# Optimization experiments

Measured on AMD Instinct MI355X. Metric: run time of the kernel, lower is better.

Reference implementation:

```python
import jax, jax.numpy as jnp
import numpy as np

KERNEL_SIZE = 128
NEG_INF = -1e30


def setup_inputs() -> dict:
    key = jax.random.key(0)
    ks = jax.random.split(key, 5)
    B, S, D, H = 4, 4096, 512, 512
    x = jax.random.normal(ks[0], (B, S, D), dtype=jnp.float32)
    # torch nn.Linear weights: [out_features, in_features], y = x @ W.T + b
    Wq_w = jax.random.normal(ks[1], (H, D), dtype=jnp.float32) * (1.0 / np.sqrt(D))
    Wq_b = jax.random.normal(ks[2], (H,), dtype=jnp.float32) * 0.01
    Wk_w = jax.random.normal(ks[3], (H, D), dtype=jnp.float32) * (1.0 / np.sqrt(D))
    Wk_b = jax.random.normal(ks[4], (H,), dtype=jnp.float32) * 0.01
    return {"x": x, "Wq_w": Wq_w, "Wq_b": Wq_b, "Wk_w": Wk_w, "Wk_b": Wk_b}


def reference(x, Wq_w, Wq_b, Wk_w, Wk_b):
    # q, k: [B, S, H]
    q = jnp.einsum('bsd,hd->bsh', x, Wq_w) + Wq_b
    k = jnp.einsum('bsd,hd->bsh', x, Wk_w) + Wk_b
    # dense scores [B, S, S]
    scores = jnp.einsum('bih,bjh->bij', q, k)
    # band mask: True where i-kernel_size+1 <= j <= i+kernel_size-1
    idx = jnp.arange(x.shape[1])
    band = jnp.abs(idx[:, None] - idx[None, :]) < KERNEL_SIZE  # [S, S]
    scores = jnp.where(band[None, :, :], scores, NEG_INF)
    attn = jax.nn.softmax(scores, axis=2)
    # attend over raw x (no V projection in original module)
    return jnp.einsum('bij,bjd->bid', attn, x)
```

## Files before the change

### kernel.cpp

```cpp
#include <hip/hip_runtime.h>
#include <hip/hip_bf16.h>

#define S_LEN 4096
#define NEG_INF_F (-1e30f)

typedef __attribute__((ext_vector_type(4))) float f32x4;
typedef __attribute__((ext_vector_type(8))) short s16x8;
typedef unsigned short u16;

static __device__ __forceinline__ u16 f2bf(float f) {
    unsigned u = __builtin_bit_cast(unsigned, f);
    unsigned r = u + 0x7FFFu + ((u >> 16) & 1u);
    return (u16)(r >> 16);
}
static __device__ __forceinline__ float bf2f(u16 h) {
    unsigned u = ((unsigned)h) << 16;
    return __builtin_bit_cast(float, u);
}
static __device__ __forceinline__ void split4(const float4 v, ushort4& hi, ushort4& lo) {
    hi.x = f2bf(v.x); lo.x = f2bf(v.x - bf2f(hi.x));
    hi.y = f2bf(v.y); lo.y = f2bf(v.y - bf2f(hi.y));
    hi.z = f2bf(v.z); lo.z = f2bf(v.z - bf2f(hi.z));
    hi.w = f2bf(v.w); lo.w = f2bf(v.w - bf2f(hi.w));
}
static __device__ __forceinline__ void gl_lds16(const void* g, void* l) {
    __builtin_amdgcn_global_load_lds(
        (const __attribute__((address_space(1))) void*)g,
        (__attribute__((address_space(3))) void*)l, 16, 0, 0);
}
static __device__ __forceinline__ int swz64(int row, int col_u16) {
    return row * 64 + (col_u16 ^ ((row & 7) << 3));
}
static __device__ __forceinline__ int swz32(int row, int col_u16) {
    return row * 32 + (col_u16 ^ (((row >> 1) & 3) << 3));
}
static __device__ __forceinline__ int swz320(int row, int col_u16) {
    return row * 320 + (col_u16 ^ ((row & 7) << 3));
}
static __device__ __forceinline__ int xcd_swz512(int bid) {
    return (bid & 7) * 64 + (bid >> 3);
}
static __device__ __forceinline__ int xcd_swz256(int bid) {
    return (bid & 7) * 32 + (bid >> 3);
}

__global__ __launch_bounds__(256) void split_xt_kernel(
    const float* __restrict__ x, u16* __restrict__ xh, u16* __restrict__ xl,
    u16* __restrict__ xT) {
    const int bid = blockIdx.x;
    const int dt = bid & 7, st = (bid >> 3) & 63, b = bid >> 9;
    const int s0 = st * 64, d0 = dt * 64;
    __shared__ u16 T[64][72];
    const int tid = threadIdx.x;
    #pragma unroll
    for (int i = 0; i < 4; ++i) {
        int idx = i * 256 + tid;
        int r = idx >> 4, c4 = (idx & 15) * 4;
        float4 v = *(const float4*)(x + (size_t)(b * S_LEN + s0 + r) * 512 + d0 + c4);
        ushort4 hi, lo; split4(v, hi, lo);
        *(ushort4*)(xh + (size_t)(b * S_LEN + s0 + r) * 512 + d0 + c4) = hi;
        *(ushort4*)(xl + (size_t)(b * S_LEN + s0 + r) * 512 + d0 + c4) = lo;
        *(ushort4*)&T[r][c4] = hi;
    }
    __syncthreads();
    #pragma unroll
    for (int i = 0; i < 2; ++i) {
        int idx = i * 256 + tid;
        int dr = idx >> 3, sc = idx & 7;
        s16x8 v;
        #pragma unroll
        for (int t = 0; t < 8; ++t) v[t] = (short)T[sc * 8 + t][dr];
        *(s16x8*)&xT[(size_t)(b * 512 + d0 + dr) * S_LEN + s0 + sc * 8] = v;
    }
}

__global__ __launch_bounds__(256) void mt_kernel(
    const float* __restrict__ Wk, const float* __restrict__ Wq,
    u16* __restrict__ Mth, u16* __restrict__ Mtl) {
    const int bm = blockIdx.x & 15, bn = blockIdx.x >> 4;
    const int m0 = bm * 32, n0 = bn * 32;
    __shared__ __align__(16) u16 Ath[32 * 72], Atl[32 * 72];
    __shared__ __align__(16) u16 Bth[32 * 72], Btl[32 * 72];
    const int tid = threadIdx.x, lane = tid & 63, w = tid >> 6;
    const int rg = w >> 1, cg = w & 1;
    const int frow = lane & 15, fk = (lane >> 4) * 8;
    f32x4 acc = {};

    for (int h0 = 0; h0 < 512; h0 += 64) {
        #pragma unroll
        for (int i = 0; i < 2; ++i) {
            int idx = i * 256 + tid;
            int h = idx >> 3, c4 = (idx & 7) * 4;
            float4 a = *(const float4*)(Wk + (size_t)(h0 + h) * 512 + m0 + c4);
            ushort4 ahi, alo; split4(a, ahi, alo);
            Ath[(c4 + 0) * 72 + h] = ahi.x; Atl[(c4 + 0) * 72 + h] = alo.x;
            Ath[(c4 + 1) * 72 + h] = ahi.y; Atl[(c4 + 1) * 72 + h] = alo.y;
            Ath[(c4 + 2) * 72 + h] = ahi.z; Atl[(c4 + 2) * 72 + h] = alo.z;
            Ath[(c4 + 3) * 72 + h] = ahi.w; Atl[(c4 + 3) * 72 + h] = alo.w;
            float4 b = *(const float4*)(Wq + (size_t)(h0 + h) * 512 + n0 + c4);
            ushort4 bhi, blo; split4(b, bhi, blo);
            Bth[(c4 + 0) * 72 + h] = bhi.x; Btl[(c4 + 0) * 72 + h] = blo.x;
            Bth[(c4 + 1) * 72 + h] = bhi.y; Btl[(c4 + 1) * 72 + h] = blo.y;
            Bth[(c4 + 2) * 72 + h] = bhi.z; Btl[(c4 + 2) * 72 + h] = blo.z;
            Bth[(c4 + 3) * 72 + h] = bhi.w; Btl[(c4 + 3) * 72 + h] = blo.w;
        }
        __syncthreads();
        #pragma unroll
        for (int kk = 0; kk < 2; ++kk) {
            s16x8 aH = *(const s16x8*)&Ath[(rg * 16 + frow) * 72 + kk * 32 + fk];
            s16x8 aL = *(const s16x8*)&Atl[(rg * 16 + frow) * 72 + kk * 32 + fk];
            s16x8 bH = *(const s16x8*)&Bth[(cg * 16 + frow) * 72 + kk * 32 + fk];
            s16x8 bL = *(const s16x8*)&Btl[(cg * 16 + frow) * 72 + kk * 32 + fk];
            acc = __builtin_amdgcn_mfma_f32_16x16x32_bf16(aH, bH, acc, 0, 0, 0);
            acc = __builtin_amdgcn_mfma_f32_16x16x32_bf16(aH, bL, acc, 0, 0, 0);
            acc = __builtin_amdgcn_mfma_f32_16x16x32_bf16(aL, bH, acc, 0, 0, 0);
        }
        __syncthreads();
    }
    {
        int d1 = n0 + cg * 16 + frow;
        #pragma unroll
        for (int e = 0; e < 4; ++e) {
            int d2 = m0 + rg * 16 + (lane >> 4) * 4 + e;
            float v = acc[e];
            u16 hi = f2bf(v);
            Mth[(size_t)d2 * 512 + d1] = hi;
            Mtl[(size_t)d2 * 512 + d1] = f2bf(v - bf2f(hi));
        }
    }
}

__global__ __launch_bounds__(256) void u_kernel(
    const float* __restrict__ Wk, const float* __restrict__ bq,
    float* __restrict__ u) {
    __shared__ float red[4][64];
    const int tid = threadIdx.x, c = tid & 63, hg = tid >> 6;
    const int d2 = blockIdx.x * 64 + c;
    float acc = 0.f;
    for (int h = hg; h < 512; h += 4) acc += Wk[(size_t)h * 512 + d2] * bq[h];
    red[hg][c] = acc;
    __syncthreads();
    if (hg == 0) u[d2] = red[0][c] + red[1][c] + red[2][c] + red[3][c];
}

__global__ __launch_bounds__(512) void z_kernel(
    const u16* __restrict__ xh, const u16* __restrict__ xl,
    const u16* __restrict__ Mth, const u16* __restrict__ Mtl,
    const float* __restrict__ u, u16* __restrict__ zh, u16* __restrict__ zl) {
    const int w_ = xcd_swz512((int)blockIdx.x);
    const int bm = w_ >> 2, bn = w_ & 3;
    const int m0 = bm * 128, n0 = bn * 128;
    __shared__ __align__(16) u16 Ah[128 * 64], Al[128 * 64];
    __shared__ __align__(16) u16 Bh[128 * 64], Bl[128 * 64];
    const int tid = threadIdx.x, lane = tid & 63, w = tid >> 6;
    const int rg = w >> 2, cg = w & 3;
    const int frow = lane & 15, fk = (lane >> 4) * 8;
    f32x4 acc[4][2] = {};

    for (int k0 = 0; k0 < 512; k0 += 64) {
        #pragma unroll
        for (int i = 0; i < 2; ++i) {
            int idx = i * 512 + tid;
            int r = idx >> 3, c = idx & 7;
            int sc = (c ^ (r & 7)) * 8;
            gl_lds16(xh + (size_t)(m0 + r) * 512 + k0 + sc, &Ah[idx * 8]);
            gl_lds16(xl + (size_t)(m0 + r) * 512 + k0 + sc, &Al[idx * 8]);
            gl_lds16(Mth + (size_t)(n0 + r) * 512 + k0 + sc, &Bh[idx * 8]);
            gl_lds16(Mtl + (size_t)(n0 + r) * 512 + k0 + sc, &Bl[idx * 8]);
        }
        __syncthreads();
        #pragma unroll
        for (int kk = 0; kk < 2; ++kk) {
            s16x8 aH[4], aL[4], bH[2], bL[2];
            #pragma unroll
            for (int mi = 0; mi < 4; ++mi) {
                int row = rg * 64 + mi * 16 + frow;
                aH[mi] = *(const s16x8*)&Ah[swz64(row, kk * 32 + fk)];
                aL[mi] = *(const s16x8*)&Al[swz64(row, kk * 32 + fk)];
            }
            #pragma unroll
            for (int ni = 0; ni < 2; ++ni) {
                int row = cg * 32 + ni * 16 + frow;
                bH[ni] = *(const s16x8*)&Bh[swz64(row, kk * 32 + fk)];
                bL[ni] = *(const s16x8*)&Bl[swz64(row, kk * 32 + fk)];
            }
            #pragma unroll
            for (int mi = 0; mi < 4; ++mi)
                #pragma unroll
                for (int ni = 0; ni < 2; ++ni) {
                    acc[mi][ni] = __builtin_amdgcn_mfma_f32_16x16x32_bf16(aH[mi], bH[ni], acc[mi][ni], 0, 0, 0);
                    acc[mi][ni] = __builtin_amdgcn_mfma_f32_16x16x32_bf16(aH[mi], bL[ni], acc[mi][ni], 0, 0, 0);
                    acc[mi][ni] = __builtin_amdgcn_mfma_f32_16x16x32_bf16(aL[mi], bH[ni], acc[mi][ni], 0, 0, 0);
                }
        }
        __syncthreads();
    }
    #pragma unroll
    for (int ni = 0; ni < 2; ++ni) {
        int col = n0 + cg * 32 + ni * 16 + frow;
        float uv = u[col];
        #pragma unroll
        for (int mi = 0; mi < 4; ++mi) {
            int rbase = m0 + rg * 64 + mi * 16 + (lane >> 4) * 4;
            #pragma unroll
            for (int e = 0; e < 4; ++e) {
                float v = acc[mi][ni][e] + uv;
                u16 hi = f2bf(v);
                zh[(size_t)(rbase + e) * 512 + col] = hi;
                zl[(size_t)(rbase + e) * 512 + col] = f2bf(v - bf2f(hi));
            }
        }
    }
}

__global__ __launch_bounds__(1024, 4) void attn_kernel(
    const u16* __restrict__ zh, const u16* __restrict__ zl,
    const u16* __restrict__ xh, const u16* __restrict__ xl,
    const u16* __restrict__ xT, float* __restrict__ out) {
    const int w_ = xcd_swz256((int)blockIdx.x);
    const int b = w_ >> 6, it = w_ & 63;
    const int i0 = it * 64, j0 = i0 - 128;
    const int mrow0 = b * S_LEN + i0;

    __shared__ __align__(16) u16 smem[40960];

    const int tid = threadIdx.x, lane = tid & 63, w = tid >> 6;
    const int g = w >> 2, q = w & 3;
    const int frow = lane & 15, fk = (lane >> 4) * 8;
    const int tstart = g + q * 4;
    const int nt = (q == 3) ? 5 : 4;
    const size_t qoff = (size_t)(mrow0 + g * 16 + frow) * 512;
    const int rq = (lane >> 4) * 4;

    f32x4 acc[5] = {};
    s16x8 krA[3], krB[3];

    auto kload = [&](int s, s16x8* kr) {
        const int k0 = s * 32;
        #pragma unroll
        for (int i = 0; i < 3; ++i) {
            int f = i * 1024 + tid;
            if (f < 2560) {
                int idx = (f < 1280) ? f : f - 1280;
                int r = idx >> 2, c = idx & 3;
                int j = min(max(j0 + r, 0), S_LEN - 1);
                const u16* src = (f < 1280) ? xh : xl;
                kr[i] = *(const s16x8*)(src + (size_t)(b * S_LEN + j) * 512 + k0 + c * 8);
            }
        }
    };
    auto kwrite = [&](const s16x8* kr, int bufoff) {
        #pragma unroll
        for (int i = 0; i < 3; ++i) {
            int f = i * 1024 + tid;
            if (f < 2560) {
                int idx = (f < 1280) ? f : f - 1280;
                int r = idx >> 2, c = idx & 3;
                int off = bufoff + ((f < 1280) ? 0 : 10240) + swz32(r, c * 8);
                *(s16x8*)&smem[off] = kr[i];
            }
        }
    };
    auto qkstep = [&](int t, int bufoff) {
        const int k0 = t * 32;
        s16x8 zH = *(const s16x8*)(zh + qoff + k0 + fk);
        s16x8 zL = *(const s16x8*)(zl + qoff + k0 + fk);
        __builtin_amdgcn_s_setprio(1);
        #pragma unroll
        for (int tt = 0; tt < 5; ++tt) {
            if (tt < nt) {
                int krow = (tstart + tt) * 16 + frow;
                s16x8 bH = *(const s16x8*)&smem[bufoff + swz32(krow, fk)];
                s16x8 bL = *(const s16x8*)&smem[bufoff + 10240 + swz32(krow, fk)];
                acc[tt] = __builtin_amdgcn_mfma_f32_16x16x32_bf16(zH, bH, acc[tt], 0, 0, 0);
                acc[tt] = __builtin_amdgcn_mfma_f32_16x16x32_bf16(zH, bL, acc[tt], 0, 0, 0);
                acc[tt] = __builtin_amdgcn_mfma_f32_16x16x32_bf16(zL, bH, acc[tt], 0, 0, 0);
            }
        }
        __builtin_amdgcn_s_setprio(0);
    };

    kload(0, krA);
    kwrite(krA, 0);
    kload(1, krB);
    __syncthreads();
    for (int tt2 = 0; tt2 < 16; tt2 += 2) {
        if (tt2 + 1 < 16) kwrite(krB, 20480);
        if (tt2 + 2 < 16) kload(tt2 + 2, krA);
        qkstep(tt2, 0);
        __syncthreads();
        if (tt2 + 1 < 16) {
            if (tt2 + 2 < 16) kwrite(krA, 0);
            if (tt2 + 3 < 16) kload(tt2 + 3, krB);
            qkstep(tt2 + 1, 20480);
            __syncthreads();
        }
    }

    float* sred_max = (float*)&smem[20480];
    float* sred_sum = sred_max + 256;
    #pragma unroll
    for (int e = 0; e < 4; ++e) {
        int r = g * 16 + rq + e;
        float m = NEG_INF_F;
        #pragma unroll
        for (int tt = 0; tt < 5; ++tt) {
            if (tt < nt) {
                int jj = (tstart + tt) * 16 + frow;
                int dj = jj - r, j = j0 + jj;
                if (dj >= 1 && dj <= 255 && j >= 0 && j < S_LEN) m = fmaxf(m, acc[tt][e]);
            }
        }
        #pragma unroll
        for (int d = 1; d < 16; d <<= 1) m = fmaxf(m, __shfl_xor(m, d));
        if (frow == 0) sred_max[r * 4 + q] = m;
    }
    __syncthreads();
    float sh[4];
    #pragma unroll
    for (int e = 0; e < 4; ++e) {
        int r = g * 16 + rq + e;
        float mx = fmaxf(fmaxf(sred_max[r * 4], sred_max[r * 4 + 1]),
                         fmaxf(sred_max[r * 4 + 2], sred_max[r * 4 + 3]));
        float s = 0.f;
        #pragma unroll
        for (int tt = 0; tt < 5; ++tt) {
            float pv = 0.f;
            if (tt < nt) {
                int jj = (tstart + tt) * 16 + frow;
                int dj = jj - r, j = j0 + jj;
                bool valid = (dj >= 1 && dj <= 255 && j >= 0 && j < S_LEN);
                pv = valid ? __expf(acc[tt][e] - mx) : 0.f;
            }
            acc[tt][e] = pv;
            s += pv;
        }
        #pragma unroll
        for (int d = 1; d < 16; d <<= 1) s += __shfl_xor(s, d);
        sh[e] = s;
    }
    if (frow == 0) {
        #pragma unroll
        for (int e = 0; e < 4; ++e) sred_sum[(g * 16 + rq + e) * 4 + q] = sh[e];
    }
    __syncthreads();
    float invv[4];
    #pragma unroll
    for (int e = 0; e < 4; ++e) {
        int r = g * 16 + rq + e;
        invv[e] = 1.f / (sred_sum[r * 4] + sred_sum[r * 4 + 1] +
                         sred_sum[r * 4 + 2] + sred_sum[r * 4 + 3]);
    }
    __syncthreads();
    #pragma unroll
    for (int tt = 0; tt < 5; ++tt) {
        if (tt < nt) {
            int t = tstart + tt;
            #pragma unroll
            for (int e = 0; e < 4; ++e) {
                int r = g * 16 + rq + e;
                smem[swz320(r, t * 16 + frow)] = f2bf(acc[tt][e] * invv[e]);
            }
        }
    }
    if (q == 0) {
        for (int t = 0; t < g; ++t)
            #pragma unroll
            for (int e = 0; e < 4; ++e)
                smem[swz320(g * 16 + rq + e, t * 16 + frow)] = 0;
    }
    if (q == 3) {
        for (int t = g + 17; t < 20; ++t)
            #pragma unroll
            for (int e = 0; e < 4; ++e)
                smem[swz320(g * 16 + rq + e, t * 16 + frow)] = 0;
    }

    s16x8 vreg[3];
    auto vload = [&](int ds) {
        const int d0 = ds * 64;
        #pragma unroll
        for (int i = 0; i < 3; ++i) {
            int f = i * 1024 + tid;
            if (f < 2560) {
                int dr = f / 40, c8 = f - dr * 40;
                int jb = j0 + c8 * 8;
                jb = min(max(jb, 0), S_LEN - 8);
                vreg[i] = *(const s16x8*)&xT[(size_t)(b * 512 + d0 + dr) * S_LEN + jb];
            }
        }
    };
    auto vwrite = [&]() {
        #pragma unroll
        for (int i = 0; i < 3; ++i) {
            int f = i * 1024 + tid;
            if (f < 2560) {
                int dr = f / 40, c8 = f - dr * 40;
                *(s16x8*)&smem[20480 + swz320(dr, c8 * 8)] = vreg[i];
            }
        }
    };
    vload(0);
    for (int ds = 0; ds < 8; ++ds) {
        __syncthreads();
        vwrite();
        __syncthreads();
        if (ds < 7) vload(ds + 1);
        f32x4 po = {};
        __builtin_amdgcn_s_setprio(1);
        #pragma unroll
        for (int jt = 0; jt < 10; ++jt) {
            s16x8 a = *(const s16x8*)&smem[swz320(g * 16 + frow, jt * 32 + fk)];
            s16x8 bv = *(const s16x8*)&smem[20480 + swz320(q * 16 + frow, jt * 32 + fk)];
            po = __builtin_amdgcn_mfma_f32_16x16x32_bf16(a, bv, po, 0, 0, 0);
        }
        __builtin_amdgcn_s_setprio(0);
        #pragma unroll
        for (int e = 0; e < 4; ++e) {
            int r = mrow0 + g * 16 + rq + e;
            out[(size_t)r * 512 + ds * 64 + q * 16 + frow] = po[e];
        }
    }
}

extern "C" void kernel_launch(void* const* d_in, const int* in_sizes, int n_in,
                              void* d_out, int out_size, void* d_ws, size_t ws_size,
                              hipStream_t stream) {
    const float* x  = (const float*)d_in[0];
    const float* Wq = (const float*)d_in[1];
    const float* bq = (const float*)d_in[2];
    const float* Wk = (const float*)d_in[3];
    const float* bk = (const float*)d_in[4];
    (void)bk;
    float* out = (float*)d_out;

    u16* xh  = (u16*)d_ws;
    u16* xl  = xh + (size_t)8388608;
    u16* zh  = xl + (size_t)8388608;
    u16* zl  = zh + (size_t)8388608;
    u16* Mth = zl + (size_t)8388608;
    u16* Mtl = Mth + (size_t)262144;
    u16* xT  = Mtl + (size_t)262144;
    float* uv = (float*)(xT + (size_t)8388608);

    hipLaunchKernelGGL(split_xt_kernel, dim3(2048), dim3(256), 0, stream, x, xh, xl, xT);
    hipLaunchKernelGGL(mt_kernel, dim3(256), dim3(256), 0, stream, Wk, Wq, Mth, Mtl);
    hipLaunchKernelGGL(u_kernel, dim3(8), dim3(256), 0, stream, Wk, bq, uv);
    hipLaunchKernelGGL(z_kernel, dim3(512), dim3(512), 0, stream,
                       xh, xl, Mth, Mtl, uv, zh, zl);
    hipLaunchKernelGGL(attn_kernel, dim3(256), dim3(1024), 0, stream,
                       zh, zl, xh, xl, xT, out);
}
```

Baseline: 140.2 us.

## Register-prefetch next K tile in z_kernel with smaller LDS footprint

Replaces the direct global-to-LDS loads of 64-wide K tiles with a register-staged pipeline over 32-wide K tiles. The next tile is fetched into registers while MFMAs run on the current one. LDS use drops to a single 32 KB buffer, and a launch-bounds occupancy hint plus setprio around the MFMA block are added. This trades twice as many loop iterations and barriers, plus extra registers for the prefetch, for overlap of global loads with compute and higher occupancy.

New measurement: 141.8 us. No clear change (+1.2%).

```diff
diff --git a/kernel.cpp b/kernel.cpp
--- a/kernel.cpp
+++ b/kernel.cpp
@@ -143,57 +143,69 @@
     if (hg == 0) u[d2] = red[0][c] + red[1][c] + red[2][c] + red[3][c];
 }
 
-__global__ __launch_bounds__(512) void z_kernel(
+__global__ __launch_bounds__(512, 4) void z_kernel(
     const u16* __restrict__ xh, const u16* __restrict__ xl,
     const u16* __restrict__ Mth, const u16* __restrict__ Mtl,
     const float* __restrict__ u, u16* __restrict__ zh, u16* __restrict__ zl) {
     const int w_ = xcd_swz512((int)blockIdx.x);
     const int bm = w_ >> 2, bn = w_ & 3;
     const int m0 = bm * 128, n0 = bn * 128;
-    __shared__ __align__(16) u16 Ah[128 * 64], Al[128 * 64];
-    __shared__ __align__(16) u16 Bh[128 * 64], Bl[128 * 64];
+    __shared__ __align__(16) u16 smz[16384];
     const int tid = threadIdx.x, lane = tid & 63, w = tid >> 6;
     const int rg = w >> 2, cg = w & 3;
     const int frow = lane & 15, fk = (lane >> 4) * 8;
     f32x4 acc[4][2] = {};
-
-    for (int k0 = 0; k0 < 512; k0 += 64) {
-        #pragma unroll
-        for (int i = 0; i < 2; ++i) {
-            int idx = i * 512 + tid;
-            int r = idx >> 3, c = idx & 7;
-            int sc = (c ^ (r & 7)) * 8;
-            gl_lds16(xh + (size_t)(m0 + r) * 512 + k0 + sc, &Ah[idx * 8]);
-            gl_lds16(xl + (size_t)(m0 + r) * 512 + k0 + sc, &Al[idx * 8]);
-            gl_lds16(Mth + (size_t)(n0 + r) * 512 + k0 + sc, &Bh[idx * 8]);
-            gl_lds16(Mtl + (size_t)(n0 + r) * 512 + k0 + sc, &Bl[idx * 8]);
-        }
-        __syncthreads();
-        #pragma unroll
-        for (int kk = 0; kk < 2; ++kk) {
-            s16x8 aH[4], aL[4], bH[2], bL[2];
+    s16x8 kr[4];
+
+    auto kload = [&](int t) {
+        const int k0 = t * 32;
+        #pragma unroll
+        for (int i = 0; i < 4; ++i) {
+            int f = i * 512 + tid;
+            int a = f >> 9, idx = f & 511;
+            int r = idx >> 2, c = idx & 3;
+            const u16* src = (a == 0) ? xh : (a == 1) ? xl : (a == 2) ? Mth : Mtl;
+            const int row0 = (a < 2) ? m0 : n0;
+            kr[i] = *(const s16x8*)(src + (size_t)(row0 + r) * 512 + k0 + c * 8);
+        }
+    };
+    auto kwrite = [&]() {
+        #pragma unroll
+        for (int i = 0; i < 4; ++i) {
+            int f = i * 512 + tid;
+            int a = f >> 9, idx = f & 511;
+            int r = idx >> 2, c = idx & 3;
+            *(s16x8*)&smz[a * 4096 + swz32(r, c * 8)] = kr[i];
+        }
+    };
+
+    kload(0);
+    for (int t = 0; t < 16; ++t) {
+        __syncthreads();
+        kwrite();
+        __syncthreads();
+        if (t < 15) kload(t + 1);
+        s16x8 aH[4], aL[4];
+        #pragma unroll
+        for (int mi = 0; mi < 4; ++mi) {
+            int row = rg * 64 + mi * 16 + frow;
+            aH[mi] = *(const s16x8*)&smz[0 * 4096 + swz32(row, fk)];
+            aL[mi] = *(const s16x8*)&smz[1 * 4096 + swz32(row, fk)];
+        }
+        __builtin_amdgcn_s_setprio(1);
+        #pragma unroll
+        for (int ni = 0; ni < 2; ++ni) {
+            int row = cg * 32 + ni * 16 + frow;
+            s16x8 bH = *(const s16x8*)&smz[2 * 4096 + swz32(row, fk)];
+            s16x8 bL = *(const s16x8*)&smz[3 * 4096 + swz32(row, fk)];
             #pragma unroll
             for (int mi = 0; mi < 4; ++mi) {
-                int row = rg * 64 + mi * 16 + frow;
-                aH[mi] = *(const s16x8*)&Ah[swz64(row, kk * 32 + fk)];
-                aL[mi] = *(const s16x8*)&Al[swz64(row, kk * 32 + fk)];
-            }
-            #pragma unroll
-            for (int ni = 0; ni < 2; ++ni) {
-                int row = cg * 32 + ni * 16 + frow;
-                bH[ni] = *(const s16x8*)&Bh[swz64(row, kk * 32 + fk)];
-                bL[ni] = *(const s16x8*)&Bl[swz64(row, kk * 32 + fk)];
-            }
-            #pragma unroll
-            for (int mi = 0; mi < 4; ++mi)
-                #pragma unroll
-                for (int ni = 0; ni < 2; ++ni) {
-                    acc[mi][ni] = __builtin_amdgcn_mfma_f32_16x16x32_bf16(aH[mi], bH[ni], acc[mi][ni], 0, 0, 0);
-                    acc[mi][ni] = __builtin_amdgcn_mfma_f32_16x16x32_bf16(aH[mi], bL[ni], acc[mi][ni], 0, 0, 0);
-                    acc[mi][ni] = __builtin_amdgcn_mfma_f32_16x16x32_bf16(aL[mi], bH[ni], acc[mi][ni], 0, 0, 0);
-                }
-        }
-        __syncthreads();
+                acc[mi][ni] = __builtin_amdgcn_mfma_f32_16x16x32_bf16(aH[mi], bH, acc[mi][ni], 0, 0, 0);
+                acc[mi][ni] = __builtin_amdgcn_mfma_f32_16x16x32_bf16(aH[mi], bL, acc[mi][ni], 0, 0, 0);
+                acc[mi][ni] = __builtin_amdgcn_mfma_f32_16x16x32_bf16(aL[mi], bH, acc[mi][ni], 0, 0, 0);
+            }
+        }
+        __builtin_amdgcn_s_setprio(0);
     }
     #pragma unroll
     for (int ni = 0; ni < 2; ++ni) {
```
